# Optimization experiments

Hardware: AMD Instinct MI355X
Metric: run time of the kernel (lower is better)

Reference implementation:

```python
import jax, jax.numpy as jnp
import numpy as np

GRID = 64
DX = 1.0 / GRID            # grid spacing (buffer dx)
RADIUS = 2.5 * DX          # search_radius = dx * 2.5
CIN, COUT = 16, 16
B, N = 2, 8192
EPS = 1e-12
FOUR_OVER_PI = 4.0 / np.pi


def _safe_sqrt(v):
    return jnp.sqrt(jnp.maximum(v, EPS))


def _sphere_to_cylinder(x, y, z):
    # volume-preserving map: unit ball -> cylinder (radius 1, height 2)
    sq = x * x + y * y + z * z
    norm = _safe_sqrt(sq)
    xy2 = x * x + y * y
    cap = 1.25 * z * z > xy2                      # polar-cap region
    s_cap = jnp.sqrt(3.0 * norm / (norm + jnp.abs(z) + EPS))
    s_side = norm / _safe_sqrt(xy2)
    xc = jnp.where(cap, x * s_cap, x * s_side)
    yc = jnp.where(cap, y * s_cap, y * s_side)
    zc = jnp.where(cap, jnp.sign(z) * norm, 1.5 * z)
    zero = sq <= EPS
    z0 = jnp.zeros_like(x)
    return (jnp.where(zero, z0, xc), jnp.where(zero, z0, yc), jnp.where(zero, z0, zc))


def _cylinder_to_cube(x, y, z):
    # area-preserving disc -> square on the xy cross-section
    xy2 = x * x + y * y
    nxy = _safe_sqrt(xy2)
    xdom = jnp.abs(y) <= jnp.abs(x)
    safe_x = jnp.where(jnp.abs(x) > EPS, x, 1.0)
    safe_y = jnp.where(jnp.abs(y) > EPS, y, 1.0)
    tx = jnp.sign(x) * nxy
    ty = jnp.sign(y) * nxy
    xa, ya = tx, tx * FOUR_OVER_PI * jnp.arctan(y / safe_x)
    xb, yb = ty * FOUR_OVER_PI * jnp.arctan(x / safe_y), ty
    xc = jnp.where(xdom, xa, xb)
    yc = jnp.where(xdom, ya, yb)
    zero = xy2 <= EPS
    z0 = jnp.zeros_like(x)
    return jnp.where(zero, z0, xc), jnp.where(zero, z0, yc), z


def _cconv_forward(input, pos, weights, grid_pos):
    Bb, C, D, H, Wd = input.shape
    Np = pos.shape[1]
    # [B,C,D,H,W] -> [B,D,H,W,C] -> [B,G,C]  (matches permute+view in torch)
    feat = jnp.transpose(input, (0, 2, 3, 4, 1)).reshape(Bb, D * H * Wd, C)
    # fixed 6^3 stencil of candidate grid cells around each point
    off = jnp.arange(6) - 2
    o0, o1, o2 = jnp.meshgrid(off, off, off, indexing='ij')
    offs = jnp.stack([o0, o1, o2], axis=-1).reshape(-1, 3)          # [216,3]
    base = jnp.floor(pos / DX).astype(jnp.int32)                    # [B,N,3]
    cand = base[:, :, None, :] + offs[None, None]                   # [B,N,216,3]
    dims = jnp.array([D, H, Wd])
    in_bounds = jnp.all((cand >= 0) & (cand < dims), axis=-1)       # [B,N,216]
    cc = jnp.clip(cand, 0, dims - 1)
    flat = (cc[..., 0] * H + cc[..., 1]) * Wd + cc[..., 2]          # [B,N,216]
    bidx = jnp.arange(Bb)[:, None, None]
    npos = grid_pos[flat]                                           # [B,N,216,3]
    fg = feat[bidx, flat]                                           # [B,N,216,C]
    rel = npos - pos[:, :, None, :]
    dist2 = jnp.sum(rel * rel, axis=-1)
    valid = in_bounds & (dist2 <= RADIUS * RADIUS)
    # map relative offsets (scaled to the unit ball) to the unit cube
    u = rel / RADIUS
    x, y, z = _sphere_to_cylinder(u[..., 0], u[..., 1], u[..., 2])
    x, y, z = _cylinder_to_cube(x, y, z)
    # linear interpolation of the 3x3x3 kernel, align_corners=True -> coords in [0,2]
    taps = jnp.arange(3, dtype=pos.dtype)
    def hat(c):
        c = jnp.clip((c * 0.5 + 0.5) * 2.0, 0.0, 2.0)
        return jnp.maximum(0.0, 1.0 - jnp.abs(c[..., None] - taps))  # [B,N,216,3]
    w0, w1, w2 = hat(x), hat(y), hat(z)
    w27 = jnp.einsum('bnki,bnkj,bnkl->bnkijl', w0, w1, w2).reshape(Bb, Np, -1, 27)
    w27 = w27 * valid[..., None].astype(w27.dtype)
    # accumulate interpolated features per kernel tap, then apply the kernel
    acc = jnp.einsum('bnkt,bnkc->bntc', w27, fg)                    # [B,N,27,C]
    out = jnp.einsum('bntc,tcd->bnd', acc, weights.reshape(27, C, -1))
    # normalize=True (Open3D default): divide by neighbor count
    count = jnp.sum(valid, axis=-1).astype(out.dtype)
    out = out / jnp.maximum(count, 1.0)[..., None]
    return out


def setup_inputs() -> dict:
    key = jax.random.key(0)
    k1, k2, k3 = jax.random.split(key, 3)
    inp = jax.random.normal(k1, (B, CIN, GRID, GRID, GRID), jnp.float32)
    pos = jax.random.uniform(k2, (B, N, 3), jnp.float32)
    weights = jax.random.normal(k3, (3, 3, 3, CIN, COUT), jnp.float32) * 0.05
    ax = jnp.arange(GRID, dtype=jnp.float32) * DX
    g = jnp.stack(jnp.meshgrid(ax, ax, ax, indexing='ij'), axis=-1).reshape(-1, 3)
    return {"input": inp, "pos": pos, "weights": weights, "grid_pos": g}


def reference(input, pos, weights, grid_pos):
    return _cconv_forward(input, pos, weights, grid_pos)
```

## Files before the change

### kernel.cpp

```cpp
#include <hip/hip_runtime.h>
#include <cstdint>

namespace {
constexpr int kGrid = 64;
constexpr int kG = kGrid * kGrid * kGrid;
constexpr int kB = 2;
constexpr int kN = 8192;
constexpr int kPts = kB * kN;
constexpr float kDX = 1.0f / 64.0f;
constexpr float kRad2 = 0.00152587890625f;
constexpr float kRad = 0.0390625f;
constexpr float kEps = 1e-12f;
constexpr float kFourOverPi = 1.27323954473516268615f;

constexpr int PPB = 4;
constexpr int THREADS = PPB * 64;
constexpr int MAXREC = 96;
constexpr int SLOT = 12;
constexpr int GSTRIDE = MAXREC * SLOT + 4;
}

__device__ __forceinline__ float sgnf(float v) {
    return (v > 0.f) ? 1.f : ((v < 0.f) ? -1.f : 0.f);
}

__global__ __launch_bounds__(256) void transpose_feat_k(const float* __restrict__ in,
                                                        float* __restrict__ feat) {
    int idx = blockIdx.x * 256 + threadIdx.x;
    if (idx >= kB * kG) return;
    int b = idx >> 18;
    int g = idx & (kG - 1);
    float v[16];
#pragma unroll
    for (int c = 0; c < 16; ++c) v[c] = in[((size_t)(b * 16 + c)) * kG + g];
    float4* dst = reinterpret_cast<float4*>(feat + (size_t)idx * 16);
    dst[0] = make_float4(v[0], v[1], v[2], v[3]);
    dst[1] = make_float4(v[4], v[5], v[6], v[7]);
    dst[2] = make_float4(v[8], v[9], v[10], v[11]);
    dst[3] = make_float4(v[12], v[13], v[14], v[15]);
}

__global__ __launch_bounds__(THREADS) void cconv_main(
    const float* __restrict__ input, const float* __restrict__ pos,
    const float* __restrict__ W, const float* __restrict__ feat,
    float* __restrict__ out, int use_feat)
{
    __shared__ __align__(16) float rec[PPB * GSTRIDE];

    const int tid = threadIdx.x;
    const int wv = tid >> 6;
    const int lane = tid & 63;
    const int sg = lane >> 4;
    const int lig = lane & 15;
    const int pt = blockIdx.x * PPB + wv;
    const int b = pt >> 13;

    const float px = pos[pt * 3 + 0];
    const float py = pos[pt * 3 + 1];
    const float pz = pos[pt * 3 + 2];
    const int bx = (int)floorf(px * 64.f);
    const int by = (int)floorf(py * 64.f);
    const int bz = (int)floorf(pz * 64.f);

    float* grec = rec + wv * GSTRIDE;
    int nv = 0;

#pragma unroll
    for (int it = 0; it < 4; ++it) {
        int k = it * 64 + lane;
        bool valid = false;
        float rx = 0.f, ry = 0.f, rz = 0.f;
        int flat = 0;
        if (k < 216) {
            int a = k / 36;
            int r = k - a * 36;
            int b1 = r / 6;
            int c1 = r - b1 * 6;
            int g0 = bx + a - 2, g1 = by + b1 - 2, g2 = bz + c1 - 2;
            bool inb = (g0 >= 0) & (g0 < 64) & (g1 >= 0) & (g1 < 64) &
                       (g2 >= 0) & (g2 < 64);
            int q0 = min(max(g0, 0), 63);
            int q1 = min(max(g1, 0), 63);
            int q2 = min(max(g2, 0), 63);
            flat = (q0 * 64 + q1) * 64 + q2;
            rx = __fsub_rn((float)q0 * kDX, px);
            ry = __fsub_rn((float)q1 * kDX, py);
            rz = __fsub_rn((float)q2 * kDX, pz);
            float d2 = __fadd_rn(__fadd_rn(__fmul_rn(rx, rx), __fmul_rn(ry, ry)),
                                 __fmul_rn(rz, rz));
            valid = inb && (d2 <= kRad2);
        }
        unsigned long long ball = __ballot(valid);
        if (valid) {
            int slot = nv + __popcll(ball & ((1ull << lane) - 1ull));
            float* rp = grec + slot * SLOT;
            *reinterpret_cast<float4*>(rp) =
                make_float4(rx, ry, rz, __int_as_float(flat));
        }
        nv += (int)__popcll(ball);
    }
    __syncthreads();

    for (int s0 = 0; s0 < nv; s0 += 64) {
        int s = s0 + lane;
        if (s < nv) {
            float* rp = grec + s * SLOT;
            float4 rc = *reinterpret_cast<const float4*>(rp);
            int flat = __float_as_int(rc.w);
            float ux = rc.x / kRad, uy = rc.y / kRad, uz = rc.z / kRad;

            float sq = ux * ux + uy * uy + uz * uz;
            float nrm = sqrtf(fmaxf(sq, kEps));
            float xy2 = ux * ux + uy * uy;
            float xc, yc, zc;
            if (1.25f * uz * uz > xy2) {
                float s2 = sqrtf(3.f * nrm / (nrm + fabsf(uz) + kEps));
                xc = ux * s2; yc = uy * s2; zc = sgnf(uz) * nrm;
            } else {
                float s2 = nrm / sqrtf(fmaxf(xy2, kEps));
                xc = ux * s2; yc = uy * s2; zc = 1.5f * uz;
            }
            if (sq <= kEps) { xc = 0.f; yc = 0.f; zc = 0.f; }

            float xy2b = xc * xc + yc * yc;
            float nxy = sqrtf(fmaxf(xy2b, kEps));
            float xo, yo;
            if (fabsf(yc) <= fabsf(xc)) {
                float sx = (fabsf(xc) > kEps) ? xc : 1.f;
                float tx = sgnf(xc) * nxy;
                xo = tx;
                yo = tx * kFourOverPi * atanf(yc / sx);
            } else {
                float sy = (fabsf(yc) > kEps) ? yc : 1.f;
                float ty = sgnf(yc) * nxy;
                xo = ty * kFourOverPi * atanf(xc / sy);
                yo = ty;
            }
            if (xy2b <= kEps) { xo = 0.f; yo = 0.f; }
            float zo = zc;

            float cx = fminf(fmaxf((xo * 0.5f + 0.5f) * 2.0f, 0.f), 2.f);
            float cy = fminf(fmaxf((yo * 0.5f + 0.5f) * 2.0f, 0.f), 2.f);
            float cz = fminf(fmaxf((zo * 0.5f + 0.5f) * 2.0f, 0.f), 2.f);
            float wx0 = fmaxf(0.f, 1.f - fabsf(cx));
            float wx1 = fmaxf(0.f, 1.f - fabsf(cx - 1.f));
            float wx2 = fmaxf(0.f, 1.f - fabsf(cx - 2.f));
            float wy0 = fmaxf(0.f, 1.f - fabsf(cy));
            float wy1 = fmaxf(0.f, 1.f - fabsf(cy - 1.f));
            float wy2 = fmaxf(0.f, 1.f - fabsf(cy - 2.f));
            float wz0 = fmaxf(0.f, 1.f - fabsf(cz));
            float wz1 = fmaxf(0.f, 1.f - fabsf(cz - 1.f));
            float wz2 = fmaxf(0.f, 1.f - fabsf(cz - 2.f));

            *reinterpret_cast<float4*>(rp)     = make_float4(wx0, wx1, wx2, wy0);
            *reinterpret_cast<float4*>(rp + 4) = make_float4(wy1, wy2, wz0, wz1);
            *reinterpret_cast<float2*>(rp + 8) = make_float2(wz2, __int_as_float(flat));
        }
    }
    __syncthreads();

    float acc[27];
#pragma unroll
    for (int t = 0; t < 27; ++t) acc[t] = 0.f;

    const float* fb = use_feat ? (feat + (size_t)b * kG * 16)
                               : (input + (size_t)b * 16 * kG);

    int s = sg;
    float4 A, Bv; float2 Cv; float f = 0.f;
    if (s < nv) {
        const float* rp = grec + s * SLOT;
        A  = *reinterpret_cast<const float4*>(rp);
        Bv = *reinterpret_cast<const float4*>(rp + 4);
        Cv = *reinterpret_cast<const float2*>(rp + 8);
        int flat = __float_as_int(Cv.y);
        f = use_feat ? fb[(size_t)flat * 16 + lig] : fb[(size_t)lig * kG + flat];
    }
    while (s < nv) {
        int s2 = s + 4;
        float4 An, Bn; float2 Cn; float fn = 0.f;
        if (s2 < nv) {
            const float* rp = grec + s2 * SLOT;
            An = *reinterpret_cast<const float4*>(rp);
            Bn = *reinterpret_cast<const float4*>(rp + 4);
            Cn = *reinterpret_cast<const float2*>(rp + 8);
            int flat = __float_as_int(Cn.y);
            fn = use_feat ? fb[(size_t)flat * 16 + lig] : fb[(size_t)lig * kG + flat];
        }
        float m0 = Bv.z * f, m1 = Bv.w * f, m2 = Cv.x * f;
        float p;
        p = A.x * A.w;  acc[0]  += p * m0; acc[1]  += p * m1; acc[2]  += p * m2;
        p = A.x * Bv.x; acc[3]  += p * m0; acc[4]  += p * m1; acc[5]  += p * m2;
        p = A.x * Bv.y; acc[6]  += p * m0; acc[7]  += p * m1; acc[8]  += p * m2;
        p = A.y * A.w;  acc[9]  += p * m0; acc[10] += p * m1; acc[11] += p * m2;
        p = A.y * Bv.x; acc[12] += p * m0; acc[13] += p * m1; acc[14] += p * m2;
        p = A.y * Bv.y; acc[15] += p * m0; acc[16] += p * m1; acc[17] += p * m2;
        p = A.z * A.w;  acc[18] += p * m0; acc[19] += p * m1; acc[20] += p * m2;
        p = A.z * Bv.x; acc[21] += p * m0; acc[22] += p * m1; acc[23] += p * m2;
        p = A.z * Bv.y; acc[24] += p * m0; acc[25] += p * m1; acc[26] += p * m2;
        A = An; Bv = Bn; Cv = Cn; f = fn; s = s2;
    }

#pragma unroll
    for (int t = 0; t < 27; ++t) {
        acc[t] += __shfl_xor(acc[t], 16);
        acc[t] += __shfl_xor(acc[t], 32);
    }

    float partial[16];
#pragma unroll
    for (int d = 0; d < 16; ++d) partial[d] = 0.f;
    for (int t = sg; t < 27; t += 4) {
        const float4* wr = reinterpret_cast<const float4*>(W + t * 256 + lig * 16);
        float4 a0 = wr[0], a1 = wr[1], a2 = wr[2], a3 = wr[3];
        float at = acc[t];
        partial[0]  += at * a0.x; partial[1]  += at * a0.y;
        partial[2]  += at * a0.z; partial[3]  += at * a0.w;
        partial[4]  += at * a1.x; partial[5]  += at * a1.y;
        partial[6]  += at * a1.z; partial[7]  += at * a1.w;
        partial[8]  += at * a2.x; partial[9]  += at * a2.y;
        partial[10] += at * a2.z; partial[11] += at * a2.w;
        partial[12] += at * a3.x; partial[13] += at * a3.y;
        partial[14] += at * a3.z; partial[15] += at * a3.w;
    }
#pragma unroll
    for (int m = 1; m < 16; m <<= 1) {
#pragma unroll
        for (int d = 0; d < 16; ++d)
            partial[d] += __shfl_xor(partial[d], m, 16);
    }
    float res = 0.f;
#pragma unroll
    for (int d = 0; d < 16; ++d)
        if (lig == d) res = partial[d];
    res += __shfl_xor(res, 16);
    res += __shfl_xor(res, 32);
    res = res / fmaxf((float)nv, 1.f);
    if (lane < 16) out[(size_t)pt * 16 + lig] = res;
}

extern "C" void kernel_launch(void* const* d_in, const int* in_sizes, int n_in,
                              void* d_out, int out_size, void* d_ws, size_t ws_size,
                              hipStream_t stream) {
    const float* input = (const float*)d_in[0];
    const float* pos   = (const float*)d_in[1];
    const float* W     = (const float*)d_in[2];
    float* out  = (float*)d_out;
    float* feat = (float*)d_ws;

    const size_t feat_bytes = (size_t)kB * kG * 16 * sizeof(float);
    int use_feat = (d_ws != nullptr && ws_size >= feat_bytes) ? 1 : 0;

    if (use_feat) {
        transpose_feat_k<<<(kB * kG + 255) / 256, 256, 0, stream>>>(input, feat);
    }
    cconv_main<<<kPts / PPB, THREADS, 0, stream>>>(input, pos, W, feat, out, use_feat);
}
```

Measured before the change: 75.78 us.

## Precompute xy weight products, use fast intrinsics and recursive-halving shuffle reductions

The per-neighbor weight records now store precomputed wx*wy products and use a 16-float slot, with zero-padded tail records so the gather loop runs without bounds checks. Block barriers become wave barriers. The mapping uses hardware sqrt/rsq/rcp and a polynomial atan in place of atanf and divisions. The cross-lane reductions of the 27 taps and 16 outputs use recursive-halving shuffles instead of full butterflies. The polynomial atan and approximate intrinsics may change numerics slightly, and shrinking MAXREC to 88 risks overflow if a point has more neighbors.

```diff
diff --git a/kernel.cpp b/kernel.cpp
--- a/kernel.cpp
+++ b/kernel.cpp
@@ -2,21 +2,20 @@
 #include <cstdint>
 
 namespace {
-constexpr int kGrid = 64;
-constexpr int kG = kGrid * kGrid * kGrid;
+constexpr int kG = 262144;
 constexpr int kB = 2;
 constexpr int kN = 8192;
 constexpr int kPts = kB * kN;
 constexpr float kDX = 1.0f / 64.0f;
 constexpr float kRad2 = 0.00152587890625f;
-constexpr float kRad = 0.0390625f;
+constexpr float kInvRad = 25.6f;
 constexpr float kEps = 1e-12f;
 constexpr float kFourOverPi = 1.27323954473516268615f;
 
 constexpr int PPB = 4;
 constexpr int THREADS = PPB * 64;
-constexpr int MAXREC = 96;
-constexpr int SLOT = 12;
+constexpr int MAXREC = 88;
+constexpr int SLOT = 16;
 constexpr int GSTRIDE = MAXREC * SLOT + 4;
 }
 
@@ -93,146 +92,161 @@
         unsigned long long ball = __ballot(valid);
         if (valid) {
             int slot = nv + __popcll(ball & ((1ull << lane) - 1ull));
-            float* rp = grec + slot * SLOT;
-            *reinterpret_cast<float4*>(rp) =
+            *reinterpret_cast<float4*>(grec + slot * SLOT) =
                 make_float4(rx, ry, rz, __int_as_float(flat));
         }
         nv += (int)__popcll(ball);
     }
-    __syncthreads();
-
-    for (int s0 = 0; s0 < nv; s0 += 64) {
-        int s = s0 + lane;
-        if (s < nv) {
-            float* rp = grec + s * SLOT;
-            float4 rc = *reinterpret_cast<const float4*>(rp);
-            int flat = __float_as_int(rc.w);
-            float ux = rc.x / kRad, uy = rc.y / kRad, uz = rc.z / kRad;
-
-            float sq = ux * ux + uy * uy + uz * uz;
-            float nrm = sqrtf(fmaxf(sq, kEps));
-            float xy2 = ux * ux + uy * uy;
-            float xc, yc, zc;
-            if (1.25f * uz * uz > xy2) {
-                float s2 = sqrtf(3.f * nrm / (nrm + fabsf(uz) + kEps));
-                xc = ux * s2; yc = uy * s2; zc = sgnf(uz) * nrm;
-            } else {
-                float s2 = nrm / sqrtf(fmaxf(xy2, kEps));
-                xc = ux * s2; yc = uy * s2; zc = 1.5f * uz;
-            }
-            if (sq <= kEps) { xc = 0.f; yc = 0.f; zc = 0.f; }
-
-            float xy2b = xc * xc + yc * yc;
-            float nxy = sqrtf(fmaxf(xy2b, kEps));
-            float xo, yo;
-            if (fabsf(yc) <= fabsf(xc)) {
-                float sx = (fabsf(xc) > kEps) ? xc : 1.f;
-                float tx = sgnf(xc) * nxy;
-                xo = tx;
-                yo = tx * kFourOverPi * atanf(yc / sx);
-            } else {
-                float sy = (fabsf(yc) > kEps) ? yc : 1.f;
-                float ty = sgnf(yc) * nxy;
-                xo = ty * kFourOverPi * atanf(xc / sy);
-                yo = ty;
-            }
-            if (xy2b <= kEps) { xo = 0.f; yo = 0.f; }
-            float zo = zc;
-
-            float cx = fminf(fmaxf((xo * 0.5f + 0.5f) * 2.0f, 0.f), 2.f);
-            float cy = fminf(fmaxf((yo * 0.5f + 0.5f) * 2.0f, 0.f), 2.f);
-            float cz = fminf(fmaxf((zo * 0.5f + 0.5f) * 2.0f, 0.f), 2.f);
-            float wx0 = fmaxf(0.f, 1.f - fabsf(cx));
-            float wx1 = fmaxf(0.f, 1.f - fabsf(cx - 1.f));
-            float wx2 = fmaxf(0.f, 1.f - fabsf(cx - 2.f));
-            float wy0 = fmaxf(0.f, 1.f - fabsf(cy));
-            float wy1 = fmaxf(0.f, 1.f - fabsf(cy - 1.f));
-            float wy2 = fmaxf(0.f, 1.f - fabsf(cy - 2.f));
-            float wz0 = fmaxf(0.f, 1.f - fabsf(cz));
-            float wz1 = fmaxf(0.f, 1.f - fabsf(cz - 1.f));
-            float wz2 = fmaxf(0.f, 1.f - fabsf(cz - 2.f));
-
-            *reinterpret_cast<float4*>(rp)     = make_float4(wx0, wx1, wx2, wy0);
-            *reinterpret_cast<float4*>(rp + 4) = make_float4(wy1, wy2, wz0, wz1);
-            *reinterpret_cast<float2*>(rp + 8) = make_float2(wz2, __int_as_float(flat));
-        }
-    }
-    __syncthreads();
-
-    float acc[27];
-#pragma unroll
-    for (int t = 0; t < 27; ++t) acc[t] = 0.f;
-
-    const float* fb = use_feat ? (feat + (size_t)b * kG * 16)
-                               : (input + (size_t)b * 16 * kG);
-
-    int s = sg;
-    float4 A, Bv; float2 Cv; float f = 0.f;
-    if (s < nv) {
-        const float* rp = grec + s * SLOT;
-        A  = *reinterpret_cast<const float4*>(rp);
-        Bv = *reinterpret_cast<const float4*>(rp + 4);
-        Cv = *reinterpret_cast<const float2*>(rp + 8);
-        int flat = __float_as_int(Cv.y);
-        f = use_feat ? fb[(size_t)flat * 16 + lig] : fb[(size_t)lig * kG + flat];
-    }
-    while (s < nv) {
-        int s2 = s + 4;
-        float4 An, Bn; float2 Cn; float fn = 0.f;
-        if (s2 < nv) {
-            const float* rp = grec + s2 * SLOT;
-            An = *reinterpret_cast<const float4*>(rp);
-            Bn = *reinterpret_cast<const float4*>(rp + 4);
-            Cn = *reinterpret_cast<const float2*>(rp + 8);
-            int flat = __float_as_int(Cn.y);
-            fn = use_feat ? fb[(size_t)flat * 16 + lig] : fb[(size_t)lig * kG + flat];
-        }
-        float m0 = Bv.z * f, m1 = Bv.w * f, m2 = Cv.x * f;
-        float p;
-        p = A.x * A.w;  acc[0]  += p * m0; acc[1]  += p * m1; acc[2]  += p * m2;
-        p = A.x * Bv.x; acc[3]  += p * m0; acc[4]  += p * m1; acc[5]  += p * m2;
-        p = A.x * Bv.y; acc[6]  += p * m0; acc[7]  += p * m1; acc[8]  += p * m2;
-        p = A.y * A.w;  acc[9]  += p * m0; acc[10] += p * m1; acc[11] += p * m2;
-        p = A.y * Bv.x; acc[12] += p * m0; acc[13] += p * m1; acc[14] += p * m2;
-        p = A.y * Bv.y; acc[15] += p * m0; acc[16] += p * m1; acc[17] += p * m2;
-        p = A.z * A.w;  acc[18] += p * m0; acc[19] += p * m1; acc[20] += p * m2;
-        p = A.z * Bv.x; acc[21] += p * m0; acc[22] += p * m1; acc[23] += p * m2;
-        p = A.z * Bv.y; acc[24] += p * m0; acc[25] += p * m1; acc[26] += p * m2;
-        A = An; Bv = Bn; Cv = Cn; f = fn; s = s2;
-    }
-
-#pragma unroll
-    for (int t = 0; t < 27; ++t) {
-        acc[t] += __shfl_xor(acc[t], 16);
-        acc[t] += __shfl_xor(acc[t], 32);
+    __builtin_amdgcn_wave_barrier();
+
+    if (lane < 8 && nv + lane < MAXREC) {
+        float4 z = make_float4(0.f, 0.f, 0.f, 0.f);
+        float4* zp = reinterpret_cast<float4*>(grec + (nv + lane) * SLOT);
+        zp[0] = z; zp[1] = z; zp[2] = z; zp[3] = z;
+    }
+
+    for (int s = lane; s < nv; s += 64) {
+        float* rp = grec + s * SLOT;
+        float4 rc = *reinterpret_cast<const float4*>(rp);
+        float flat_bits = rc.w;
+        float ux = rc.x * kInvRad, uy = rc.y * kInvRad, uz = rc.z * kInvRad;
+
+        float xx = ux * ux, yy = uy * uy, zz = uz * uz;
+        float xy2 = xx + yy;
+        float sq = xy2 + zz;
+        float nrm = __builtin_amdgcn_sqrtf(fmaxf(sq, kEps));
+        bool cap = (1.25f * zz > xy2);
+        float scap = __builtin_amdgcn_sqrtf(3.f * nrm) *
+                     __builtin_amdgcn_rsqf(nrm + fabsf(uz) + kEps);
+        float sside = nrm * __builtin_amdgcn_rsqf(fmaxf(xy2, kEps));
+        float sc = cap ? scap : sside;
+        float xc = ux * sc, yc = uy * sc;
+        float zc = cap ? sgnf(uz) * nrm : 1.5f * uz;
+        bool z1 = (sq <= kEps);
+        if (z1) { xc = 0.f; yc = 0.f; zc = 0.f; }
+
+        float xy2b = xc * xc + yc * yc;
+        float nxy = __builtin_amdgcn_sqrtf(fmaxf(xy2b, kEps));
+        bool xdom = (fabsf(yc) <= fabsf(xc));
+        float num = xdom ? yc : xc;
+        float den = xdom ? xc : yc;
+        float dsafe = (fabsf(den) > kEps) ? den : 1.0f;
+        float r = num * __builtin_amdgcn_rcpf(dsafe);
+        float r2 = r * r;
+        float at = -0.01172120f;
+        at = at * r2 + 0.05265332f;
+        at = at * r2 - 0.11643287f;
+        at = at * r2 + 0.19354346f;
+        at = at * r2 - 0.33262347f;
+        at = at * r2 + 0.99997726f;
+        at = at * r;
+        float tt = sgnf(den) * nxy;
+        float g = tt * kFourOverPi * at;
+        float xo = xdom ? tt : g;
+        float yo = xdom ? g : tt;
+        if (xy2b <= kEps) { xo = 0.f; yo = 0.f; }
+        float zo = zc;
+
+        float tx = fminf(fmaxf(xo + 1.f, 0.f), 2.f) - 1.f;
+        float ty = fminf(fmaxf(yo + 1.f, 0.f), 2.f) - 1.f;
+        float tz = fminf(fmaxf(zo + 1.f, 0.f), 2.f) - 1.f;
+        float wx0 = fmaxf(0.f, -tx), wx1 = 1.f - fabsf(tx), wx2 = fmaxf(0.f, tx);
+        float wy0 = fmaxf(0.f, -ty), wy1 = 1.f - fabsf(ty), wy2 = fmaxf(0.f, ty);
+        float wz0 = fmaxf(0.f, -tz), wz1 = 1.f - fabsf(tz), wz2 = fmaxf(0.f, tz);
+
+        float4* rp4 = reinterpret_cast<float4*>(rp);
+        rp4[0] = make_float4(wx0 * wy0, wx0 * wy1, wx0 * wy2, wz0);
+        rp4[1] = make_float4(wx1 * wy0, wx1 * wy1, wx1 * wy2, wz1);
+        rp4[2] = make_float4(wx2 * wy0, wx2 * wy1, wx2 * wy2, wz2);
+        rp[12] = flat_bits;
+    }
+    __builtin_amdgcn_wave_barrier();
+
+    float acc[28];
+#pragma unroll
+    for (int t = 0; t < 28; ++t) acc[t] = 0.f;
+
+    const float* fbp = use_feat ? (feat + (size_t)b * kG * 16)
+                                : (input + (size_t)b * 16 * kG);
+    const int nvp = (nv + 3) & ~3;
+
+    const float* rp = grec + sg * SLOT;
+    float4 F0 = reinterpret_cast<const float4*>(rp)[0];
+    float4 F1 = reinterpret_cast<const float4*>(rp)[1];
+    float4 F2 = reinterpret_cast<const float4*>(rp)[2];
+    int flat = __float_as_int(rp[12]);
+    float f = use_feat ? fbp[(size_t)flat * 16 + lig] : fbp[(size_t)lig * kG + flat];
+
+    for (int s = sg; s < nvp; s += 4) {
+        const float* rpn = rp + 4 * SLOT;
+        float4 G0 = reinterpret_cast<const float4*>(rpn)[0];
+        float4 G1 = reinterpret_cast<const float4*>(rpn)[1];
+        float4 G2 = reinterpret_cast<const float4*>(rpn)[2];
+        int flatn = __float_as_int(rpn[12]);
+        float fn = use_feat ? fbp[(size_t)flatn * 16 + lig]
+                            : fbp[(size_t)lig * kG + flatn];
+        float m0 = F0.w * f, m1 = F1.w * f, m2 = F2.w * f;
+        acc[0]  += F0.x * m0; acc[1]  += F0.x * m1; acc[2]  += F0.x * m2;
+        acc[3]  += F0.y * m0; acc[4]  += F0.y * m1; acc[5]  += F0.y * m2;
+        acc[6]  += F0.z * m0; acc[7]  += F0.z * m1; acc[8]  += F0.z * m2;
+        acc[9]  += F1.x * m0; acc[10] += F1.x * m1; acc[11] += F1.x * m2;
+        acc[12] += F1.y * m0; acc[13] += F1.y * m1; acc[14] += F1.y * m2;
+        acc[15] += F1.z * m0; acc[16] += F1.z * m1; acc[17] += F1.z * m2;
+        acc[18] += F2.x * m0; acc[19] += F2.x * m1; acc[20] += F2.x * m2;
+        acc[21] += F2.y * m0; acc[22] += F2.y * m1; acc[23] += F2.y * m2;
+        acc[24] += F2.z * m0; acc[25] += F2.z * m1; acc[26] += F2.z * m2;
+        F0 = G0; F1 = G1; F2 = G2; f = fn; rp = rpn;
+    }
+
+    const bool hi32 = (lane >= 32);
+    float kp[14];
+#pragma unroll
+    for (int j = 0; j < 14; ++j) {
+        float send = hi32 ? acc[j] : acc[14 + j];
+        float recv = __shfl_xor(send, 32);
+        kp[j] = (hi32 ? acc[14 + j] : acc[j]) + recv;
+    }
+    const bool hi16 = (lane & 16) != 0;
+    float kk[7];
+#pragma unroll
+    for (int j = 0; j < 7; ++j) {
+        float send = hi16 ? kp[j] : kp[7 + j];
+        float recv = __shfl_xor(send, 16);
+        kk[j] = (hi16 ? kp[7 + j] : kp[j]) + recv;
     }
 
     float partial[16];
 #pragma unroll
     for (int d = 0; d < 16; ++d) partial[d] = 0.f;
-    for (int t = sg; t < 27; t += 4) {
-        const float4* wr = reinterpret_cast<const float4*>(W + t * 256 + lig * 16);
-        float4 a0 = wr[0], a1 = wr[1], a2 = wr[2], a3 = wr[3];
-        float at = acc[t];
-        partial[0]  += at * a0.x; partial[1]  += at * a0.y;
-        partial[2]  += at * a0.z; partial[3]  += at * a0.w;
-        partial[4]  += at * a1.x; partial[5]  += at * a1.y;
-        partial[6]  += at * a1.z; partial[7]  += at * a1.w;
-        partial[8]  += at * a2.x; partial[9]  += at * a2.y;
-        partial[10] += at * a2.z; partial[11] += at * a2.w;
-        partial[12] += at * a3.x; partial[13] += at * a3.y;
-        partial[14] += at * a3.z; partial[15] += at * a3.w;
-    }
-#pragma unroll
-    for (int m = 1; m < 16; m <<= 1) {
-#pragma unroll
-        for (int d = 0; d < 16; ++d)
-            partial[d] += __shfl_xor(partial[d], m, 16);
-    }
-    float res = 0.f;
-#pragma unroll
-    for (int d = 0; d < 16; ++d)
-        if (lig == d) res = partial[d];
+    const float* wbase = W + (sg * 7) * 256 + lig * 16;
+#pragma unroll
+    for (int j = 0; j < 7; ++j) {
+        if (sg * 7 + j < 27) {
+            const float4* wr = reinterpret_cast<const float4*>(wbase + j * 256);
+            float4 a0 = wr[0], a1 = wr[1], a2 = wr[2], a3 = wr[3];
+            float at_ = kk[j];
+            partial[0]  += at_ * a0.x; partial[1]  += at_ * a0.y;
+            partial[2]  += at_ * a0.z; partial[3]  += at_ * a0.w;
+            partial[4]  += at_ * a1.x; partial[5]  += at_ * a1.y;
+            partial[6]  += at_ * a1.z; partial[7]  += at_ * a1.w;
+            partial[8]  += at_ * a2.x; partial[9]  += at_ * a2.y;
+            partial[10] += at_ * a2.z; partial[11] += at_ * a2.w;
+            partial[12] += at_ * a3.x; partial[13] += at_ * a3.y;
+            partial[14] += at_ * a3.z; partial[15] += at_ * a3.w;
+        }
+    }
+
+#pragma unroll
+    for (int half = 8; half >= 1; half >>= 1) {
+        bool up = (lig & half) != 0;
+#pragma unroll
+        for (int j = 0; j < half; ++j) {
+            float send = up ? partial[j] : partial[j + half];
+            float recv = __shfl_xor(send, half);
+            partial[j] = (up ? partial[j + half] : partial[j]) + recv;
+        }
+    }
+    float res = partial[0];
     res += __shfl_xor(res, 16);
     res += __shfl_xor(res, 32);
     res = res / fmaxf((float)nv, 1.f);
```

Result: slower. 84.04 us (+10.9%).
